# Performance work log

Hardware: AMD Instinct MI355X
Metric: run time of the kernel (lower is better)

## Reference

```python
import jax, jax.numpy as jnp
import numpy as np

MARGIN = 0.3
NEG_FALLBACK = 1e6  # value used when a row has no negatives


def setup_inputs() -> dict:
    key = jax.random.key(0)
    k1, k2 = jax.random.split(key)
    N, D, NUM_IDS = 8192, 256, 512
    feat = jax.random.normal(k1, (N, D), dtype=jnp.float32)
    labels = jax.random.randint(k2, (N,), 0, NUM_IDS, dtype=jnp.int64)
    return {"feat": feat, "labels": labels}


def reference(feat, labels):
    N = feat.shape[0]
    sq_norms = jnp.sum(feat * feat, axis=1)  # [N]
    sq = sq_norms[:, None] + sq_norms[None, :] - 2.0 * (feat @ feat.T)  # [N,N]
    sq = jnp.maximum(sq, 0.0)
    # safe sqrt (zero distance on the diagonal would otherwise give nan grads)
    dist = jnp.where(sq > 0, jnp.sqrt(jnp.where(sq > 0, sq, 1.0)), 0.0)

    same = labels[:, None] == labels[None, :]          # [N,N] bool
    eye = jnp.eye(N, dtype=bool)
    is_pos = same & ~eye                                # exclude self-pair
    is_neg = ~same

    # hard mining: per-row masked max over positives / min over negatives
    dist_ap = jnp.where(is_pos.any(axis=1),
                        jnp.where(is_pos, dist, -jnp.inf).max(axis=1), 0.0)
    dist_an = jnp.where(is_neg.any(axis=1),
                        jnp.where(is_neg, dist, jnp.inf).min(axis=1), NEG_FALLBACK)

    # MarginRankingLoss with y=1: mean(relu(margin - (dist_an - dist_ap)))
    return jnp.mean(jnp.maximum(0.0, MARGIN + dist_ap - dist_an))
```

## Files before the change

kernel.cpp:

```cpp
#include <hip/hip_runtime.h>


constexpr int N = 8192;
constexpr int D = 256;
constexpr float MARGIN = 0.3f;
constexpr float NEG_FALLBACK = 1e6f;
constexpr float TBIG = 1e30f;

typedef __attribute__((ext_vector_type(8))) __bf16 bf16x8;
typedef __attribute__((ext_vector_type(4))) float f32x4;

__device__ __forceinline__ unsigned enc_f(float f) {
  unsigned u = __float_as_uint(f);
  return (u >> 31) ? ~u : (u | 0x80000000u);
}
__device__ __forceinline__ float dec_f(unsigned e) {
  unsigned u = (e >> 31) ? (e ^ 0x80000000u) : ~e;
  return __uint_as_float(u);
}
__device__ __forceinline__ unsigned short f2bf_rtn(float x) {
  unsigned u = __float_as_uint(x);
  return (unsigned short)((u + 0x7fffu + ((u >> 16) & 1u)) >> 16);
}


__global__ __launch_bounds__(1024)
void tl_sortk(const int* __restrict__ labels, int* __restrict__ perm,
              int* __restrict__ labp, int* __restrict__ offg) {
  __shared__ int hist[512];
  __shared__ int wsum[8];
  __shared__ int wbase[8];
  const int tid = threadIdx.x;
  const int lane = tid & 63;
  const int w = tid >> 6;
  if (tid < 512) hist[tid] = 0;
  __syncthreads();
  int l8[8];
#pragma unroll
  for (int k = 0; k < 8; ++k) {
    l8[k] = labels[tid + k * 1024];
    atomicAdd(&hist[l8[k]], 1);
  }
  __syncthreads();
  int v = 0, sc = 0;
  if (tid < 512) {
    v = hist[tid];
    sc = v;
#pragma unroll
    for (int d = 1; d < 64; d <<= 1) {
      int t = __shfl_up(sc, d, 64);
      if (lane >= d) sc += t;
    }
    if (lane == 63) wsum[w] = sc;
  }
  __syncthreads();
  if (tid == 0) {
    int a = 0;
#pragma unroll
    for (int i = 0; i < 8; ++i) { wbase[i] = a; a += wsum[i]; }
  }
  __syncthreads();
  if (tid < 512) {
    const int excl = wbase[w] + sc - v;
    offg[tid] = excl;
    hist[tid] = excl;
  }
  if (tid == 0) offg[512] = N;
  __syncthreads();
#pragma unroll
  for (int k = 0; k < 8; ++k) {
    const int pos = atomicAdd(&hist[l8[k]], 1);
    perm[pos] = tid + k * 1024;
    labp[pos] = l8[k];
  }
}


__global__ void tl_pass0p(const float* __restrict__ feat, const int* __restrict__ perm,
                          float* __restrict__ norms, unsigned* __restrict__ ap,
                          unsigned* __restrict__ an, unsigned short* __restrict__ P,
                          float* __restrict__ out) {
  const int p = blockIdx.x * 4 + (threadIdx.x >> 6);
  const int lane = threadIdx.x & 63;
  const int src = perm[p];
  float4 f = reinterpret_cast<const float4*>(feat + (size_t)src * D)[lane];
  ushort4 h;
  h.x = f2bf_rtn(f.x); h.y = f2bf_rtn(f.y); h.z = f2bf_rtn(f.z); h.w = f2bf_rtn(f.w);
  reinterpret_cast<ushort4*>(P + (size_t)p * D)[lane] = h;
  float s = fmaf(f.x, f.x, fmaf(f.y, f.y, fmaf(f.z, f.z, f.w * f.w)));
#pragma unroll
  for (int off = 32; off > 0; off >>= 1) s += __shfl_down(s, off, 64);
  if (lane == 0) {
    norms[p] = s;
    ap[p] = enc_f(-TBIG);
    an[p] = enc_f(TBIG);
  }
  if (p == 0 && lane == 0) out[0] = 0.0f;
}


__global__ __launch_bounds__(256, 2)
void tl_pass1s(const unsigned short* __restrict__ P, const int* __restrict__ labp,
               const float* __restrict__ norms, const int* __restrict__ offg,
               unsigned* __restrict__ ap, unsigned* __restrict__ an) {
  __shared__ unsigned short lB[2][128][64];

  const int tid = threadIdx.x;
  const int wave = tid >> 6;
  const int lane = tid & 63;
  const int c = lane & 15;
  const int q = lane >> 4;
  const int i0 = blockIdx.y * 128;
  const int j0 = blockIdx.x * 256;
  const int wrow = i0 + wave * 32;

  const int lo = offg[labp[i0]];
  const int hi = offg[labp[i0 + 127] + 1];

  bf16x8 af[2][8];
#pragma unroll
  for (int a = 0; a < 2; ++a)
#pragma unroll
    for (int t2 = 0; t2 < 8; ++t2)
      af[a][t2] = *(const bf16x8*)(P + (size_t)(wrow + a * 16 + c) * D + t2 * 32 + q * 8);

  f32x4 acc[2][8];
#pragma unroll
  for (int a = 0; a < 2; ++a)
#pragma unroll
    for (int b = 0; b < 8; ++b) acc[a][b] = (f32x4){0.f, 0.f, 0.f, 0.f};

  float vp[2][4], vn[2][4];
#pragma unroll
  for (int a = 0; a < 2; ++a)
#pragma unroll
    for (int r = 0; r < 4; ++r) { vp[a][r] = -TBIG; vn[a][r] = TBIG; }

  const int rsub = lane >> 3;
  const int g7 = lane & 7;

#define STAGE(BUF, JT, KC)                                                              \
  do {                                                                                  \
    const int jb_ = j0 + (JT) * 128;                                                    \
    _Pragma("unroll") for (int t = 0; t < 4; ++t) {                                     \
      const int rA_ = wave * 32 + t * 8;                                                \
      const int sg_ = g7 ^ rsub;                                                        \
      const unsigned short* gp_ = P + (size_t)(jb_ + rA_ + rsub) * D + (KC) + sg_ * 8;  \
      __builtin_amdgcn_global_load_lds(                                                 \
          (const __attribute__((address_space(1))) void*)gp_,                           \
          (__attribute__((address_space(3))) void*)&lB[BUF][rA_][0], 16, 0, 0);         \
    }                                                                                   \
  } while (0)

  STAGE(0, 0, 0);
  __syncthreads();

#pragma unroll
  for (int s = 0; s < 8; ++s) {
    const int jt = s >> 2;
    const int kk = s & 3;
    if (s < 7) STAGE((s + 1) & 1, (s + 1) >> 2, ((s + 1) & 3) * 64);

#pragma unroll
    for (int ks = 0; ks < 2; ++ks) {
      const int gsel = ((ks * 4 + q) ^ (c & 7)) * 8;
      bf16x8 bfr[8];
#pragma unroll
      for (int b = 0; b < 8; ++b)
        bfr[b] = *(const bf16x8*)&lB[s & 1][b * 16 + c][gsel];
#pragma unroll
      for (int a = 0; a < 2; ++a)
#pragma unroll
        for (int b = 0; b < 8; ++b)
          acc[a][b] = __builtin_amdgcn_mfma_f32_16x16x32_bf16(
              af[a][kk * 2 + ks], bfr[b], acc[a][b], 0, 0, 0);
    }

    if (kk == 3) {
      const int jb0 = j0 + jt * 128;
      const bool careful = (jb0 < hi) && (jb0 + 128 > lo);
      if (!careful) {
#pragma unroll
        for (int b = 0; b < 8; ++b) {
          const float njb = norms[jb0 + b * 16 + c];
#pragma unroll
          for (int a = 0; a < 2; ++a)
#pragma unroll
            for (int r = 0; r < 4; ++r)
              vn[a][r] = fminf(vn[a][r], fmaf(-2.f, acc[a][b][r], njb));
        }
      } else {
        int lj[8], cj[8];
        float nj[8];
#pragma unroll
        for (int b = 0; b < 8; ++b) {
          cj[b] = jb0 + b * 16 + c;
          nj[b] = norms[cj[b]];
          lj[b] = labp[cj[b]];
        }
#pragma unroll
        for (int a = 0; a < 2; ++a)
#pragma unroll
          for (int r = 0; r < 4; ++r) {
            const int rg = wrow + a * 16 + q * 4 + r;
            const int li = labp[rg];
            float vpl = vp[a][r], vnl = vn[a][r];
#pragma unroll
            for (int b = 0; b < 8; ++b) {
              const float t = fmaf(-2.f, acc[a][b][r], nj[b]);
              const bool sm = (lj[b] == li);
              const bool dg = (cj[b] == rg);
              vpl = fmaxf(vpl, (sm && !dg) ? t : -TBIG);
              vnl = fminf(vnl, sm ? TBIG : t);
            }
            vp[a][r] = vpl;
            vn[a][r] = vnl;
          }
      }
#pragma unroll
      for (int a = 0; a < 2; ++a)
#pragma unroll
        for (int b = 0; b < 8; ++b) acc[a][b] = (f32x4){0.f, 0.f, 0.f, 0.f};
    }
    __syncthreads();
  }
#undef STAGE

#pragma unroll
  for (int a = 0; a < 2; ++a)
#pragma unroll
    for (int r = 0; r < 4; ++r) {
      float p = vp[a][r], n = vn[a][r];
#pragma unroll
      for (int m = 1; m < 16; m <<= 1) {
        p = fmaxf(p, __shfl_xor(p, m, 64));
        n = fminf(n, __shfl_xor(n, m, 64));
      }
      if (c == 0) {
        const int rg = wrow + a * 16 + q * 4 + r;
        atomicMax(&ap[rg], enc_f(p));
        atomicMin(&an[rg], enc_f(n));
      }
    }
}


__global__ void tl_pass2f(const unsigned* __restrict__ ap, const unsigned* __restrict__ an,
                          const float* __restrict__ norms, float* __restrict__ out) {
  int r = blockIdx.x * 256 + threadIdx.x;
  float ni = norms[r];
  float tpv = dec_f(ap[r]);
  float tnv = dec_f(an[r]);
  float dap = (tpv < -1e29f) ? 0.f : sqrtf(fmaxf(ni + tpv, 0.f));
  float dan = (tnv > 1e29f) ? NEG_FALLBACK : sqrtf(fmaxf(ni + tnv, 0.f));
  float v = fmaxf(0.f, MARGIN + dap - dan) * (1.0f / (float)N);
#pragma unroll
  for (int off = 32; off > 0; off >>= 1) v += __shfl_down(v, off, 64);
  __shared__ float red[4];
  int lane = threadIdx.x & 63, w = threadIdx.x >> 6;
  if (lane == 0) red[w] = v;
  __syncthreads();
  if (threadIdx.x == 0) atomicAdd(out, red[0] + red[1] + red[2] + red[3]);
}


constexpr int FB_BK = 32;
constexpr int FB_JSPLIT = 8;
constexpr int FB_JRANGE = N / FB_JSPLIT;
constexpr int FB_LDS = 132;

__global__ void tl_pass0_fb(const float* __restrict__ feat, float* __restrict__ norms,
                            float* __restrict__ ap, float* __restrict__ an,
                            float* __restrict__ out) {
  int row = blockIdx.x * 4 + (threadIdx.x >> 6);
  int lane = threadIdx.x & 63;
  float4 f = reinterpret_cast<const float4*>(feat + (size_t)row * D)[lane];
  float s = f.x * f.x + f.y * f.y + f.z * f.z + f.w * f.w;
#pragma unroll
  for (int off = 32; off > 0; off >>= 1) s += __shfl_down(s, off, 64);
  if (lane == 0) { norms[row] = s; ap[row] = 0.0f; an[row] = NEG_FALLBACK; }
  if (row == 0 && lane == 0) out[0] = 0.0f;
}

__global__ __launch_bounds__(256, 2)
void tl_pass1_fb(const float* __restrict__ feat, const int* __restrict__ labels,
                 const float* __restrict__ norms,
                 unsigned int* __restrict__ ap, unsigned int* __restrict__ an) {
  __shared__ float As[FB_BK][FB_LDS];
  __shared__ float Bs[FB_BK][FB_LDS];
  const int tid = threadIdx.x;
  const int tx = tid & 15, ty = tid >> 4;
  const int ib0 = blockIdx.y * 128;
  const int jbase = blockIdx.x * FB_JRANGE;
  float ni[8]; int li[8]; int ri[8];
#pragma unroll
  for (int a = 0; a < 8; ++a) {
    int r = ty * 4 + (a & 3) + ((a >> 2) << 6);
    ri[a] = ib0 + r; ni[a] = norms[ri[a]]; li[a] = labels[ri[a]];
  }
  float apv[8], anv[8];
#pragma unroll
  for (int a = 0; a < 8; ++a) { apv[a] = 0.0f; anv[a] = NEG_FALLBACK; }
  for (int jt = 0; jt < FB_JRANGE; jt += 128) {
    const int jb = jbase + jt;
    float acc[8][8];
#pragma unroll
    for (int a = 0; a < 8; ++a)
#pragma unroll
      for (int b = 0; b < 8; ++b) acc[a][b] = 0.0f;
    for (int kc = 0; kc < D; kc += FB_BK) {
#pragma unroll
      for (int u = 0; u < 4; ++u) {
        int lin = tid + u * 256;
        int row = lin >> 3, c4 = lin & 7;
        float4 va = *reinterpret_cast<const float4*>(feat + (size_t)(ib0 + row) * D + kc + c4 * 4);
        As[c4 * 4 + 0][row] = va.x; As[c4 * 4 + 1][row] = va.y;
        As[c4 * 4 + 2][row] = va.z; As[c4 * 4 + 3][row] = va.w;
        float4 vb = *reinterpret_cast<const float4*>(feat + (size_t)(jb + row) * D + kc + c4 * 4);
        Bs[c4 * 4 + 0][row] = vb.x; Bs[c4 * 4 + 1][row] = vb.y;
        Bs[c4 * 4 + 2][row] = vb.z; Bs[c4 * 4 + 3][row] = vb.w;
      }
      __syncthreads();
#pragma unroll 8
      for (int k = 0; k < FB_BK; ++k) {
        float4 a0 = *reinterpret_cast<const float4*>(&As[k][ty * 4]);
        float4 a1 = *reinterpret_cast<const float4*>(&As[k][64 + ty * 4]);
        float4 b0 = *reinterpret_cast<const float4*>(&Bs[k][tx * 4]);
        float4 b1 = *reinterpret_cast<const float4*>(&Bs[k][64 + tx * 4]);
        float av[8] = {a0.x, a0.y, a0.z, a0.w, a1.x, a1.y, a1.z, a1.w};
        float bv[8] = {b0.x, b0.y, b0.z, b0.w, b1.x, b1.y, b1.z, b1.w};
#pragma unroll
        for (int a = 0; a < 8; ++a)
#pragma unroll
          for (int b = 0; b < 8; ++b) acc[a][b] = fmaf(av[a], bv[b], acc[a][b]);
      }
      __syncthreads();
    }
#pragma unroll
    for (int b = 0; b < 8; ++b) {
      int cjx = jb + tx * 4 + (b & 3) + ((b >> 2) << 6);
      float njx = norms[cjx]; int ljx = labels[cjx];
#pragma unroll
      for (int a = 0; a < 8; ++a) {
        float sq = fmaxf(ni[a] + njx - 2.0f * acc[a][b], 0.0f);
        float dist = sqrtf(sq);
        if (li[a] == ljx) { if (ri[a] != cjx) apv[a] = fmaxf(apv[a], dist); }
        else anv[a] = fminf(anv[a], dist);
      }
    }
  }
  __syncthreads();
  float* red = &As[0][0];
#pragma unroll
  for (int a = 0; a < 8; ++a) {
    int r = ty * 4 + (a & 3) + ((a >> 2) << 6);
    red[r * 16 + tx] = apv[a];
  }
  __syncthreads();
  if (tid < 128) {
    float m = red[tid * 16];
#pragma unroll
    for (int t = 1; t < 16; ++t) m = fmaxf(m, red[tid * 16 + t]);
    atomicMax(&ap[ib0 + tid], __float_as_uint(m));
  }
  __syncthreads();
#pragma unroll
  for (int a = 0; a < 8; ++a) {
    int r = ty * 4 + (a & 3) + ((a >> 2) << 6);
    red[r * 16 + tx] = anv[a];
  }
  __syncthreads();
  if (tid < 128) {
    float m = red[tid * 16];
#pragma unroll
    for (int t = 1; t < 16; ++t) m = fminf(m, red[tid * 16 + t]);
    atomicMin(&an[ib0 + tid], __float_as_uint(m));
  }
}

__global__ void tl_pass2_fb(const float* __restrict__ ap, const float* __restrict__ an,
                            float* __restrict__ out) {
  int r = blockIdx.x * 256 + threadIdx.x;
  float v = fmaxf(0.0f, MARGIN + ap[r] - an[r]) * (1.0f / (float)N);
#pragma unroll
  for (int off = 32; off > 0; off >>= 1) v += __shfl_down(v, off, 64);
  __shared__ float red[4];
  int lane = threadIdx.x & 63, w = threadIdx.x >> 6;
  if (lane == 0) red[w] = v;
  __syncthreads();
  if (threadIdx.x == 0) atomicAdd(out, red[0] + red[1] + red[2] + red[3]);
}


extern "C" void kernel_launch(void* const* d_in, const int* in_sizes, int n_in,
                              void* d_out, int out_size, void* d_ws, size_t ws_size,
                              hipStream_t stream) {
  const float* feat = (const float*)d_in[0];
  const int* labels = (const int*)d_in[1];
  float* out = (float*)d_out;

  float* norms = (float*)d_ws;
  unsigned* ap = (unsigned*)(norms + N);
  unsigned* an = ap + N;
  int* perm = (int*)(an + N);
  int* labp = perm + N;
  int* offg = labp + N;
  unsigned short* P = (unsigned short*)(offg + 520);
  const size_t NEED = (size_t)5 * N * 4 + 520 * 4 + (size_t)N * D * 2;

  if (ws_size >= NEED) {
    tl_sortk<<<1, 1024, 0, stream>>>(labels, perm, labp, offg);
    tl_pass0p<<<N / 4, 256, 0, stream>>>(feat, perm, norms, ap, an, P, out);
    dim3 grid1(32, N / 128);
    tl_pass1s<<<grid1, 256, 0, stream>>>(P, labp, norms, offg, ap, an);
    tl_pass2f<<<N / 256, 256, 0, stream>>>(ap, an, norms, out);
  } else {
    float* apf = (float*)ap;
    float* anf = (float*)an;
    tl_pass0_fb<<<N / 4, 256, 0, stream>>>(feat, norms, apf, anf, out);
    dim3 grid1(FB_JSPLIT, N / 128);
    tl_pass1_fb<<<grid1, 256, 0, stream>>>(feat, labels, norms, (unsigned*)apf, (unsigned*)anf);
    tl_pass2_fb<<<N / 256, 256, 0, stream>>>(apf, anf, out);
  }
}
```

Before: 135.4 us.

## Exploit distance-matrix symmetry by computing only upper-triangular tiles

Replaces the full N×N tile sweep with a symmetric schedule. Each block computes one 128×128 tile (i≤j) via a round-robin pairing, and both row-wise and column-wise min/max results come from the same tile. Column reductions go through shared memory and extra atomics, which roughly halves the MFMA work. The K loop changes to a triple-buffered LDS pipeline with explicit waitcnt/barriers, and column norms and labels are cached in shared memory. In exchange there are more atomics, extra per-element column reduction ALU work, and 128-column tiles per block instead of 256.

```diff
diff --git a/kernel.cpp b/kernel.cpp
--- a/kernel.cpp
+++ b/kernel.cpp
@@ -100,66 +100,98 @@
 
 
 __global__ __launch_bounds__(256, 2)
-void tl_pass1s(const unsigned short* __restrict__ P, const int* __restrict__ labp,
+void tl_pass1t(const unsigned short* __restrict__ P, const int* __restrict__ labp,
                const float* __restrict__ norms, const int* __restrict__ offg,
                unsigned* __restrict__ ap, unsigned* __restrict__ an) {
-  __shared__ unsigned short lB[2][128][64];
+  __shared__ unsigned short lB[3][128][64];
+  __shared__ float nrmS[128];
+  __shared__ int lblS[128];
+  __shared__ float colSn[4][128];
+  __shared__ float colSp[4][128];
+
+  const int g = blockIdx.x;
+  const int rr = blockIdx.y;
+  if (g < 32 && rr == 63) return;
+
+  int ti, tj;
+  if (g == 32) {
+    ti = rr; tj = rr;
+  } else if (g == 0) {
+    ti = rr; tj = 63;
+  } else {
+    const int a1 = (rr + g) % 63;
+    const int b1 = (rr - g + 63) % 63;
+    ti = a1 < b1 ? a1 : b1;
+    tj = a1 < b1 ? b1 : a1;
+  }
+  const bool diag = (g == 32);
 
   const int tid = threadIdx.x;
   const int wave = tid >> 6;
   const int lane = tid & 63;
   const int c = lane & 15;
   const int q = lane >> 4;
-  const int i0 = blockIdx.y * 128;
-  const int j0 = blockIdx.x * 256;
+  const int i0 = ti * 128;
+  const int jb0 = tj * 128;
   const int wrow = i0 + wave * 32;
 
   const int lo = offg[labp[i0]];
   const int hi = offg[labp[i0 + 127] + 1];
-
-  bf16x8 af[2][8];
-#pragma unroll
-  for (int a = 0; a < 2; ++a)
-#pragma unroll
-    for (int t2 = 0; t2 < 8; ++t2)
-      af[a][t2] = *(const bf16x8*)(P + (size_t)(wrow + a * 16 + c) * D + t2 * 32 + q * 8);
-
-  f32x4 acc[2][8];
-#pragma unroll
-  for (int a = 0; a < 2; ++a)
-#pragma unroll
-    for (int b = 0; b < 8; ++b) acc[a][b] = (f32x4){0.f, 0.f, 0.f, 0.f};
-
-  float vp[2][4], vn[2][4];
-#pragma unroll
-  for (int a = 0; a < 2; ++a)
-#pragma unroll
-    for (int r = 0; r < 4; ++r) { vp[a][r] = -TBIG; vn[a][r] = TBIG; }
+  const bool careful = (jb0 < hi) && (jb0 + 128 > lo);
 
   const int rsub = lane >> 3;
   const int g7 = lane & 7;
 
-#define STAGE(BUF, JT, KC)                                                              \
+#define STAGE(BUF, KC)                                                                  \
   do {                                                                                  \
-    const int jb_ = j0 + (JT) * 128;                                                    \
     _Pragma("unroll") for (int t = 0; t < 4; ++t) {                                     \
       const int rA_ = wave * 32 + t * 8;                                                \
-      const int sg_ = g7 ^ rsub;                                                        \
-      const unsigned short* gp_ = P + (size_t)(jb_ + rA_ + rsub) * D + (KC) + sg_ * 8;  \
+      const unsigned short* gp_ =                                                       \
+          P + (size_t)(jb0 + rA_ + rsub) * D + (KC) + (g7 ^ rsub) * 8;                  \
       __builtin_amdgcn_global_load_lds(                                                 \
           (const __attribute__((address_space(1))) void*)gp_,                           \
           (__attribute__((address_space(3))) void*)&lB[BUF][rA_][0], 16, 0, 0);         \
     }                                                                                   \
   } while (0)
 
-  STAGE(0, 0, 0);
-  __syncthreads();
-
-#pragma unroll
-  for (int s = 0; s < 8; ++s) {
-    const int jt = s >> 2;
-    const int kk = s & 3;
-    if (s < 7) STAGE((s + 1) & 1, (s + 1) >> 2, ((s + 1) & 3) * 64);
+  STAGE(0, 0);
+
+  bf16x8 af[2][8];
+#pragma unroll
+  for (int a = 0; a < 2; ++a)
+#pragma unroll
+    for (int t2 = 0; t2 < 8; ++t2)
+      af[a][t2] = *(const bf16x8*)(P + (size_t)(wrow + a * 16 + c) * D + t2 * 32 + q * 8);
+
+  int lrow[2][4];
+  float nrow[2][4];
+#pragma unroll
+  for (int a = 0; a < 2; ++a)
+#pragma unroll
+    for (int r2 = 0; r2 < 4; ++r2) {
+      const int rg = wrow + a * 16 + q * 4 + r2;
+      lrow[a][r2] = labp[rg];
+      nrow[a][r2] = norms[rg];
+    }
+
+  if (tid < 128) {
+    nrmS[tid] = norms[jb0 + tid];
+    lblS[tid] = labp[jb0 + tid];
+  }
+
+  STAGE(1, 64);
+  asm volatile("s_waitcnt vmcnt(4) lgkmcnt(0)" ::: "memory");
+  __builtin_amdgcn_s_barrier();
+
+  f32x4 acc[2][8];
+#pragma unroll
+  for (int a = 0; a < 2; ++a)
+#pragma unroll
+    for (int b = 0; b < 8; ++b) acc[a][b] = (f32x4){0.f, 0.f, 0.f, 0.f};
+
+#pragma unroll
+  for (int s = 0; s < 4; ++s) {
+    if (s < 2) STAGE((s + 2) % 3, (s + 2) * 64);
 
 #pragma unroll
     for (int ks = 0; ks < 2; ++ks) {
@@ -167,81 +199,125 @@
       bf16x8 bfr[8];
 #pragma unroll
       for (int b = 0; b < 8; ++b)
-        bfr[b] = *(const bf16x8*)&lB[s & 1][b * 16 + c][gsel];
+        bfr[b] = *(const bf16x8*)&lB[s % 3][b * 16 + c][gsel];
 #pragma unroll
       for (int a = 0; a < 2; ++a)
 #pragma unroll
         for (int b = 0; b < 8; ++b)
           acc[a][b] = __builtin_amdgcn_mfma_f32_16x16x32_bf16(
-              af[a][kk * 2 + ks], bfr[b], acc[a][b], 0, 0, 0);
-    }
-
-    if (kk == 3) {
-      const int jb0 = j0 + jt * 128;
-      const bool careful = (jb0 < hi) && (jb0 + 128 > lo);
-      if (!careful) {
+              af[a][s * 2 + ks], bfr[b], acc[a][b], 0, 0, 0);
+    }
+
+    if (s < 2) {
+      asm volatile("s_waitcnt vmcnt(4)" ::: "memory");
+      __builtin_amdgcn_s_barrier();
+    } else if (s == 2) {
+      asm volatile("s_waitcnt vmcnt(0)" ::: "memory");
+      __builtin_amdgcn_s_barrier();
+    }
+  }
+#undef STAGE
+
+  float vp[2][4], vn[2][4];
+#pragma unroll
+  for (int a = 0; a < 2; ++a)
+#pragma unroll
+    for (int r2 = 0; r2 < 4; ++r2) { vp[a][r2] = -TBIG; vn[a][r2] = TBIG; }
+  float cnb[8], cpb[8];
+#pragma unroll
+  for (int b = 0; b < 8; ++b) { cnb[b] = TBIG; cpb[b] = -TBIG; }
+
+  if (!careful) {
+#pragma unroll
+    for (int b = 0; b < 8; ++b) {
+      const float njb = nrmS[b * 16 + c];
+      float cmin = cnb[b];
+#pragma unroll
+      for (int a = 0; a < 2; ++a)
+#pragma unroll
+        for (int r2 = 0; r2 < 4; ++r2) {
+          vn[a][r2] = fminf(vn[a][r2], fmaf(-2.f, acc[a][b][r2], njb));
+          cmin = fminf(cmin, fmaf(-2.f, acc[a][b][r2], nrow[a][r2]));
+        }
+      cnb[b] = cmin;
+    }
+  } else {
+    int lj[8], cj[8];
+    float nj[8];
+#pragma unroll
+    for (int b = 0; b < 8; ++b) {
+      cj[b] = jb0 + b * 16 + c;
+      nj[b] = nrmS[b * 16 + c];
+      lj[b] = lblS[b * 16 + c];
+    }
+#pragma unroll
+    for (int a = 0; a < 2; ++a)
+#pragma unroll
+      for (int r2 = 0; r2 < 4; ++r2) {
+        const int rg = wrow + a * 16 + q * 4 + r2;
+        const int li = lrow[a][r2];
+        const float ni = nrow[a][r2];
+        float vpl = vp[a][r2], vnl = vn[a][r2];
 #pragma unroll
         for (int b = 0; b < 8; ++b) {
-          const float njb = norms[jb0 + b * 16 + c];
-#pragma unroll
-          for (int a = 0; a < 2; ++a)
-#pragma unroll
-            for (int r = 0; r < 4; ++r)
-              vn[a][r] = fminf(vn[a][r], fmaf(-2.f, acc[a][b][r], njb));
+          const float d = acc[a][b][r2];
+          const float trow = fmaf(-2.f, d, nj[b]);
+          const float tcol = fmaf(-2.f, d, ni);
+          const bool sm = (lj[b] == li);
+          const bool dg = (cj[b] == rg);
+          vpl = fmaxf(vpl, (sm && !dg) ? trow : -TBIG);
+          vnl = fminf(vnl, sm ? TBIG : trow);
+          cpb[b] = fmaxf(cpb[b], (sm && !dg) ? tcol : -TBIG);
+          cnb[b] = fminf(cnb[b], sm ? TBIG : tcol);
         }
-      } else {
-        int lj[8], cj[8];
-        float nj[8];
-#pragma unroll
-        for (int b = 0; b < 8; ++b) {
-          cj[b] = jb0 + b * 16 + c;
-          nj[b] = norms[cj[b]];
-          lj[b] = labp[cj[b]];
-        }
-#pragma unroll
-        for (int a = 0; a < 2; ++a)
-#pragma unroll
-          for (int r = 0; r < 4; ++r) {
-            const int rg = wrow + a * 16 + q * 4 + r;
-            const int li = labp[rg];
-            float vpl = vp[a][r], vnl = vn[a][r];
-#pragma unroll
-            for (int b = 0; b < 8; ++b) {
-              const float t = fmaf(-2.f, acc[a][b][r], nj[b]);
-              const bool sm = (lj[b] == li);
-              const bool dg = (cj[b] == rg);
-              vpl = fmaxf(vpl, (sm && !dg) ? t : -TBIG);
-              vnl = fminf(vnl, sm ? TBIG : t);
-            }
-            vp[a][r] = vpl;
-            vn[a][r] = vnl;
-          }
-      }
-#pragma unroll
-      for (int a = 0; a < 2; ++a)
-#pragma unroll
-        for (int b = 0; b < 8; ++b) acc[a][b] = (f32x4){0.f, 0.f, 0.f, 0.f};
-    }
-    __syncthreads();
-  }
-#undef STAGE
+        vp[a][r2] = vpl;
+        vn[a][r2] = vnl;
+      }
+  }
 
 #pragma unroll
   for (int a = 0; a < 2; ++a)
 #pragma unroll
-    for (int r = 0; r < 4; ++r) {
-      float p = vp[a][r], n = vn[a][r];
+    for (int r2 = 0; r2 < 4; ++r2) {
+      float p = vp[a][r2], n = vn[a][r2];
 #pragma unroll
       for (int m = 1; m < 16; m <<= 1) {
         p = fmaxf(p, __shfl_xor(p, m, 64));
         n = fminf(n, __shfl_xor(n, m, 64));
       }
       if (c == 0) {
-        const int rg = wrow + a * 16 + q * 4 + r;
+        const int rg = wrow + a * 16 + q * 4 + r2;
         atomicMax(&ap[rg], enc_f(p));
         atomicMin(&an[rg], enc_f(n));
       }
     }
+
+  if (!diag) {
+#pragma unroll
+    for (int b = 0; b < 8; ++b) {
+      float n = cnb[b];
+      n = fminf(n, __shfl_xor(n, 16, 64));
+      n = fminf(n, __shfl_xor(n, 32, 64));
+      if (q == 0) colSn[wave][b * 16 + c] = n;
+      if (careful) {
+        float p = cpb[b];
+        p = fmaxf(p, __shfl_xor(p, 16, 64));
+        p = fmaxf(p, __shfl_xor(p, 32, 64));
+        if (q == 0) colSp[wave][b * 16 + c] = p;
+      }
+    }
+    __syncthreads();
+    if (tid < 128) {
+      const float mn = fminf(fminf(colSn[0][tid], colSn[1][tid]),
+                             fminf(colSn[2][tid], colSn[3][tid]));
+      atomicMin(&an[jb0 + tid], enc_f(mn));
+      if (careful) {
+        const float mx = fmaxf(fmaxf(colSp[0][tid], colSp[1][tid]),
+                               fmaxf(colSp[2][tid], colSp[3][tid]));
+        atomicMax(&ap[jb0 + tid], enc_f(mx));
+      }
+    }
+  }
 }
 
 
@@ -411,8 +487,8 @@
   if (ws_size >= NEED) {
     tl_sortk<<<1, 1024, 0, stream>>>(labels, perm, labp, offg);
     tl_pass0p<<<N / 4, 256, 0, stream>>>(feat, perm, norms, ap, an, P, out);
-    dim3 grid1(32, N / 128);
-    tl_pass1s<<<grid1, 256, 0, stream>>>(P, labp, norms, offg, ap, an);
+    dim3 grid1(33, 64);
+    tl_pass1t<<<grid1, 256, 0, stream>>>(P, labp, norms, offg, ap, an);
     tl_pass2f<<<N / 256, 256, 0, stream>>>(ap, an, norms, out);
   } else {
     float* apf = (float*)ap;
```

Measured after the change: 121.3 us. -10.4%, faster.
